# Performance work log

Measured on AMD Instinct MI355X. Metric: run time of the kernel, lower is better.

## Reference

```python
import jax, jax.numpy as jnp
import numpy as np

HEAD_SIZE = 128
ROTARY_DIM = 128
BASE = 10000.0
MAX_POS = 32768
NUM_TOKENS = 8192
NUM_HEADS = 32
NUM_KV_HEADS = 8


def setup_inputs() -> dict:
    key = jax.random.key(0)
    k0, k1, k2, k3 = jax.random.split(key, 4)
    qkv_dim = (NUM_HEADS + 2 * NUM_KV_HEADS) * HEAD_SIZE  # 6144
    qkv = jax.random.normal(k0, (NUM_TOKENS, qkv_dim), dtype=jnp.float32)
    q_weight = jax.random.uniform(k1, (HEAD_SIZE,), dtype=jnp.float32)
    k_weight = jax.random.uniform(k2, (HEAD_SIZE,), dtype=jnp.float32)
    positions = jax.random.randint(k3, (NUM_TOKENS,), 0, MAX_POS)
    return {
        "qkv": qkv,
        "q_weight": q_weight,
        "k_weight": k_weight,
        "positions": positions,
        "num_heads": NUM_HEADS,
        "num_kv_heads": NUM_KV_HEADS,
        "eps": 1e-6,
    }


def _rmsnorm(x, w, eps):
    # per-head RMSNorm over head_size, computed in fp32
    xf = x.astype(jnp.float32)
    inv = jax.lax.rsqrt(jnp.mean(xf * xf, axis=-1, keepdims=True) + eps)
    return (xf * inv * w.astype(jnp.float32)).astype(x.dtype)


def _rope_neox(x, cos, sin):
    # x: [T, H, rotary_dim]; cos/sin: [T, 1, rotary_dim//2]
    half = ROTARY_DIM // 2
    x1, x2 = x[..., :half], x[..., half:]
    return jnp.concatenate([x1 * cos - x2 * sin, x2 * cos + x1 * sin], axis=-1)


def reference(qkv, q_weight, k_weight, positions, num_heads, num_kv_heads, eps):
    T = qkv.shape[0]
    nq, nk = num_heads, num_kv_heads
    q = qkv[:, : nq * HEAD_SIZE].reshape(T, nq, HEAD_SIZE)
    k = qkv[:, nq * HEAD_SIZE : (nq + nk) * HEAD_SIZE].reshape(T, nk, HEAD_SIZE)
    v = qkv[:, (nq + nk) * HEAD_SIZE :]  # untouched

    # position-indexed cos/sin (equivalent to gathering from the cache)
    inv_freq = 1.0 / (BASE ** (jnp.arange(0, ROTARY_DIM, 2, dtype=jnp.float32) / ROTARY_DIM))
    freqs = positions.astype(jnp.float32)[:, None] * inv_freq  # [T, rotary_dim//2]
    cos = jnp.cos(freqs).astype(qkv.dtype)[:, None, :]
    sin = jnp.sin(freqs).astype(qkv.dtype)[:, None, :]

    q = _rope_neox(_rmsnorm(q, q_weight, eps), cos, sin)
    k = _rope_neox(_rmsnorm(k, k_weight, eps), cos, sin)

    return jnp.concatenate([q.reshape(T, -1), k.reshape(T, -1), v], axis=-1)
```

## Files before the change

### kernel.cpp

```cpp
#include <hip/hip_runtime.h>


namespace {

constexpr int kNumQ = 32;
constexpr int kNumK = 8;
constexpr int kHead = 128;
constexpr int kRow  = (kNumQ + 2 * kNumK) * kHead;
constexpr int kHalf = 64;
constexpr int kQK   = kNumQ + kNumK;

__global__ __launch_bounds__(256) void rope_qknorm_kernel(
    const float* __restrict__ qkv,
    const float* __restrict__ qw,
    const float* __restrict__ kw,
    const int* __restrict__ positions,
    float* __restrict__ out) {
  const int t   = blockIdx.x;
  const int tid = threadIdx.x;

  __shared__ float s_cos[kHalf];
  __shared__ float s_sin[kHalf];

  if (tid < kHalf) {
    const double log2b = 13.287712379549449629;
    float p = (float)exp2((double)tid * (log2b / 64.0));
    float inv_freq = 1.0f / p;
    float phase = (float)positions[t] * inv_freq;
    const double two_pi = 6.283185307179586476925286766559;
    float pr = (float)fmod((double)phase, two_pi);
    s_cos[tid] = cosf(pr);
    s_sin[tid] = sinf(pr);
  }
  __syncthreads();

  const int g = tid >> 4;
  const int l = tid & 15;

  const float* row  = qkv + (size_t)t * kRow;
  float*       orow = out + (size_t)t * kRow;

  const float4 cz = *reinterpret_cast<const float4*>(&s_cos[l * 4]);
  const float4 sz = *reinterpret_cast<const float4*>(&s_sin[l * 4]);

  const float4 qw1 = *reinterpret_cast<const float4*>(qw + l * 4);
  const float4 qw2 = *reinterpret_cast<const float4*>(qw + kHalf + l * 4);
  const float4 kw1 = *reinterpret_cast<const float4*>(kw + l * 4);
  const float4 kw2 = *reinterpret_cast<const float4*>(kw + kHalf + l * 4);

  #pragma unroll
  for (int hb = 0; hb < 48; hb += 16) {
    const int h = hb + g;
    const float* hp = row + h * kHead + l * 4;
    const float4 a = *reinterpret_cast<const float4*>(hp);
    const float4 b = *reinterpret_cast<const float4*>(hp + kHalf);
    float* op = orow + h * kHead + l * 4;

    if (h < kQK) {
      const bool isQ = (h < kNumQ);
      const float4 w1 = isQ ? qw1 : kw1;
      const float4 w2 = isQ ? qw2 : kw2;

      float ss = a.x * a.x + a.y * a.y + a.z * a.z + a.w * a.w +
                 b.x * b.x + b.y * b.y + b.z * b.z + b.w * b.w;
      #pragma unroll
      for (int m = 1; m < 16; m <<= 1) ss += __shfl_xor(ss, m, 16);
      const float inv = rsqrtf(ss * (1.0f / 128.0f) + 1e-6f);

      const float y1x = a.x * inv * w1.x, y1y = a.y * inv * w1.y;
      const float y1z = a.z * inv * w1.z, y1w = a.w * inv * w1.w;
      const float y2x = b.x * inv * w2.x, y2y = b.y * inv * w2.y;
      const float y2z = b.z * inv * w2.z, y2w = b.w * inv * w2.w;

      float4 o1, o2;
      o1.x = y1x * cz.x - y2x * sz.x;
      o1.y = y1y * cz.y - y2y * sz.y;
      o1.z = y1z * cz.z - y2z * sz.z;
      o1.w = y1w * cz.w - y2w * sz.w;
      o2.x = y2x * cz.x + y1x * sz.x;
      o2.y = y2y * cz.y + y1y * sz.y;
      o2.z = y2z * cz.z + y1z * sz.z;
      o2.w = y2w * cz.w + y1w * sz.w;
      *reinterpret_cast<float4*>(op)         = o1;
      *reinterpret_cast<float4*>(op + kHalf) = o2;
    } else {
      *reinterpret_cast<float4*>(op)         = a;
      *reinterpret_cast<float4*>(op + kHalf) = b;
    }
  }
}

}

extern "C" void kernel_launch(void* const* d_in, const int* in_sizes, int n_in,
                              void* d_out, int out_size, void* d_ws, size_t ws_size,
                              hipStream_t stream) {
  const float* qkv     = (const float*)d_in[0];
  const float* qw      = (const float*)d_in[1];
  const float* kw      = (const float*)d_in[2];
  const int* positions = (const int*)d_in[3];
  float* out           = (float*)d_out;

  const int tokens = in_sizes[3];
  rope_qknorm_kernel<<<tokens, 256, 0, stream>>>(qkv, qw, kw, positions, out);
}
```

Measured before the change: 339.2 us.

## Precompute RoPE cos/sin table in separate kernel and use persistent grid-stride main kernel

Moves the per-token cos/sin computation out of the main kernel into a separate table kernel that uses all 256 threads per block, and replaces the fmod-based range reduction with a rintf-based one. The main kernel now reads cos/sin from the workspace table with no shared memory or block barrier, and runs as a fixed 2048-block grid looping over tokens. This removes the serialized double-precision trig prologue from every block of the memory-bound kernel. In exchange it adds a second launch, extra table traffic, and hardcodes the token count to 8192.

```diff
diff --git a/kernel.cpp b/kernel.cpp
--- a/kernel.cpp
+++ b/kernel.cpp
@@ -9,83 +9,89 @@
 constexpr int kRow  = (kNumQ + 2 * kNumK) * kHead;
 constexpr int kHalf = 64;
 constexpr int kQK   = kNumQ + kNumK;
+constexpr int kTokens = 8192;
 
-__global__ __launch_bounds__(256) void rope_qknorm_kernel(
+__global__ __launch_bounds__(256) void rope_table_kernel(
+    const int* __restrict__ positions,
+    float* __restrict__ cos_tab,
+    float* __restrict__ sin_tab) {
+  const int idx = blockIdx.x * blockDim.x + threadIdx.x;
+  if (idx >= kTokens * kHalf) return;
+  const int t = idx >> 6;
+  const int i = idx & 63;
+  const double log2b = 13.287712379549449629;
+  const float p = (float)exp2((double)i * (log2b / 64.0));
+  const float inv_freq = 1.0f / p;
+  const float phase = (float)positions[t] * inv_freq;
+  const float k = rintf(phase * 0.15915494309189535f);
+  const double r = (double)phase - (double)k * 6.283185307179586476925287;
+  const float pr = (float)r;
+  cos_tab[idx] = cosf(pr);
+  sin_tab[idx] = sinf(pr);
+}
+
+__global__ __launch_bounds__(256) void rope_main_kernel(
     const float* __restrict__ qkv,
     const float* __restrict__ qw,
     const float* __restrict__ kw,
-    const int* __restrict__ positions,
+    const float* __restrict__ cos_tab,
+    const float* __restrict__ sin_tab,
     float* __restrict__ out) {
-  const int t   = blockIdx.x;
   const int tid = threadIdx.x;
-
-  __shared__ float s_cos[kHalf];
-  __shared__ float s_sin[kHalf];
-
-  if (tid < kHalf) {
-    const double log2b = 13.287712379549449629;
-    float p = (float)exp2((double)tid * (log2b / 64.0));
-    float inv_freq = 1.0f / p;
-    float phase = (float)positions[t] * inv_freq;
-    const double two_pi = 6.283185307179586476925286766559;
-    float pr = (float)fmod((double)phase, two_pi);
-    s_cos[tid] = cosf(pr);
-    s_sin[tid] = sinf(pr);
-  }
-  __syncthreads();
-
   const int g = tid >> 4;
   const int l = tid & 15;
-
-  const float* row  = qkv + (size_t)t * kRow;
-  float*       orow = out + (size_t)t * kRow;
-
-  const float4 cz = *reinterpret_cast<const float4*>(&s_cos[l * 4]);
-  const float4 sz = *reinterpret_cast<const float4*>(&s_sin[l * 4]);
 
   const float4 qw1 = *reinterpret_cast<const float4*>(qw + l * 4);
   const float4 qw2 = *reinterpret_cast<const float4*>(qw + kHalf + l * 4);
   const float4 kw1 = *reinterpret_cast<const float4*>(kw + l * 4);
   const float4 kw2 = *reinterpret_cast<const float4*>(kw + kHalf + l * 4);
 
-  #pragma unroll
-  for (int hb = 0; hb < 48; hb += 16) {
-    const int h = hb + g;
-    const float* hp = row + h * kHead + l * 4;
-    const float4 a = *reinterpret_cast<const float4*>(hp);
-    const float4 b = *reinterpret_cast<const float4*>(hp + kHalf);
-    float* op = orow + h * kHead + l * 4;
+  for (int t = blockIdx.x; t < kTokens; t += gridDim.x) {
+    const float* row  = qkv + (size_t)t * kRow;
+    float*       orow = out + (size_t)t * kRow;
 
-    if (h < kQK) {
-      const bool isQ = (h < kNumQ);
-      const float4 w1 = isQ ? qw1 : kw1;
-      const float4 w2 = isQ ? qw2 : kw2;
+    const float4 cz = *reinterpret_cast<const float4*>(cos_tab + t * kHalf + l * 4);
+    const float4 sz = *reinterpret_cast<const float4*>(sin_tab + t * kHalf + l * 4);
 
-      float ss = a.x * a.x + a.y * a.y + a.z * a.z + a.w * a.w +
-                 b.x * b.x + b.y * b.y + b.z * b.z + b.w * b.w;
-      #pragma unroll
-      for (int m = 1; m < 16; m <<= 1) ss += __shfl_xor(ss, m, 16);
-      const float inv = rsqrtf(ss * (1.0f / 128.0f) + 1e-6f);
+    #pragma unroll
+    for (int hb = 0; hb < 48; hb += 16) {
+      const int h = hb + g;
+      const float* hp = row + h * kHead + l * 4;
+      const float4 a = *reinterpret_cast<const float4*>(hp);
+      const float4 b = *reinterpret_cast<const float4*>(hp + kHalf);
+      float* op = orow + h * kHead + l * 4;
 
-      const float y1x = a.x * inv * w1.x, y1y = a.y * inv * w1.y;
-      const float y1z = a.z * inv * w1.z, y1w = a.w * inv * w1.w;
-      const float y2x = b.x * inv * w2.x, y2y = b.y * inv * w2.y;
-      const float y2z = b.z * inv * w2.z, y2w = b.w * inv * w2.w;
+      if (h < kQK) {
+        const bool isQ = (h < kNumQ);
+        const float4 w1 = isQ ? qw1 : kw1;
+        const float4 w2 = isQ ? qw2 : kw2;
 
-      float4 o1, o2;
-      o1.x = y1x * cz.x - y2x * sz.x;
-      o1.y = y1y * cz.y - y2y * sz.y;
-      o1.z = y1z * cz.z - y2z * sz.z;
-      o1.w = y1w * cz.w - y2w * sz.w;
-      o2.x = y2x * cz.x + y1x * sz.x;
-      o2.y = y2y * cz.y + y1y * sz.y;
-      o2.z = y2z * cz.z + y1z * sz.z;
-      o2.w = y2w * cz.w + y1w * sz.w;
-      *reinterpret_cast<float4*>(op)         = o1;
-      *reinterpret_cast<float4*>(op + kHalf) = o2;
-    } else {
-      *reinterpret_cast<float4*>(op)         = a;
-      *reinterpret_cast<float4*>(op + kHalf) = b;
+        float ss = a.x * a.x + a.y * a.y + a.z * a.z + a.w * a.w +
+                   b.x * b.x + b.y * b.y + b.z * b.z + b.w * b.w;
+        #pragma unroll
+        for (int m = 1; m < 16; m <<= 1) ss += __shfl_xor(ss, m, 16);
+        const float inv = rsqrtf(ss * (1.0f / 128.0f) + 1e-6f);
+
+        const float y1x = a.x * inv * w1.x, y1y = a.y * inv * w1.y;
+        const float y1z = a.z * inv * w1.z, y1w = a.w * inv * w1.w;
+        const float y2x = b.x * inv * w2.x, y2y = b.y * inv * w2.y;
+        const float y2z = b.z * inv * w2.z, y2w = b.w * inv * w2.w;
+
+        float4 o1, o2;
+        o1.x = y1x * cz.x - y2x * sz.x;
+        o1.y = y1y * cz.y - y2y * sz.y;
+        o1.z = y1z * cz.z - y2z * sz.z;
+        o1.w = y1w * cz.w - y2w * sz.w;
+        o2.x = y2x * cz.x + y1x * sz.x;
+        o2.y = y2y * cz.y + y1y * sz.y;
+        o2.z = y2z * cz.z + y1z * sz.z;
+        o2.w = y2w * cz.w + y1w * sz.w;
+        *reinterpret_cast<float4*>(op)         = o1;
+        *reinterpret_cast<float4*>(op + kHalf) = o2;
+      } else {
+        *reinterpret_cast<float4*>(op)         = a;
+        *reinterpret_cast<float4*>(op + kHalf) = b;
+      }
     }
   }
 }
@@ -101,6 +107,12 @@
   const int* positions = (const int*)d_in[3];
   float* out           = (float*)d_out;
 
-  const int tokens = in_sizes[3];
-  rope_qknorm_kernel<<<tokens, 256, 0, stream>>>(qkv, qw, kw, positions, out);
+  float* cos_tab = (float*)d_ws;
+  float* sin_tab = cos_tab + (size_t)kTokens * kHalf;
+
+  const int table_elems = kTokens * kHalf;
+  rope_table_kernel<<<(table_elems + 255) / 256, 256, 0, stream>>>(
+      positions, cos_tab, sin_tab);
+
+  rope_main_kernel<<<2048, 256, 0, stream>>>(qkv, qw, kw, cos_tab, sin_tab, out);
 }
```

New measurement: 352.3 us. 3.9% more time.

## Process four tokens per block, cheaper phase reduction, nontemporal stores

Applied to the files above, without the earlier changes.

Each block now handles four tokens, so all 256 threads compute cos/sin for four tokens in parallel and the weight loads are amortised. The double-precision fmod is replaced by an rint-based range reduction with a single double multiply-subtract. Outputs are written with nontemporal stores to avoid polluting cache. Fewer blocks means less parallelism per block launch, and the new reduction may differ slightly in accuracy for large phases.

```diff
diff --git a/kernel.cpp b/kernel.cpp
--- a/kernel.cpp
+++ b/kernel.cpp
@@ -9,39 +9,50 @@
 constexpr int kRow  = (kNumQ + 2 * kNumK) * kHead;
 constexpr int kHalf = 64;
 constexpr int kQK   = kNumQ + kNumK;
+constexpr int kTPB  = 4;
+
+typedef float f32x4 __attribute__((ext_vector_type(4)));
+
+__device__ __forceinline__ void nt_store4(float* p, float x, float y, float z,
+                                          float w) {
+  f32x4 v;
+  v.x = x; v.y = y; v.z = z; v.w = w;
+  __builtin_nontemporal_store(v, reinterpret_cast<f32x4*>(p));
+}
 
 __global__ __launch_bounds__(256) void rope_qknorm_kernel(
     const float* __restrict__ qkv,
     const float* __restrict__ qw,
     const float* __restrict__ kw,
     const int* __restrict__ positions,
-    float* __restrict__ out) {
-  const int t   = blockIdx.x;
+    float* __restrict__ out,
+    int tokens) {
   const int tid = threadIdx.x;
+  const int t0  = blockIdx.x * kTPB;
 
-  __shared__ float s_cos[kHalf];
-  __shared__ float s_sin[kHalf];
+  __shared__ float s_cos[kTPB][kHalf];
+  __shared__ float s_sin[kTPB][kHalf];
 
-  if (tid < kHalf) {
-    const double log2b = 13.287712379549449629;
-    float p = (float)exp2((double)tid * (log2b / 64.0));
-    float inv_freq = 1.0f / p;
-    float phase = (float)positions[t] * inv_freq;
-    const double two_pi = 6.283185307179586476925286766559;
-    float pr = (float)fmod((double)phase, two_pi);
-    s_cos[tid] = cosf(pr);
-    s_sin[tid] = sinf(pr);
+  {
+    const int tl = tid >> 6;
+    const int i  = tid & 63;
+    const int t  = t0 + tl;
+    if (t < tokens) {
+      const double log2b = 13.287712379549449629;
+      const float p = (float)exp2((double)i * (log2b / 64.0));
+      const float inv_freq = 1.0f / p;
+      const float phase = (float)positions[t] * inv_freq;
+      const float k = rintf(phase * 0.15915494309189535f);
+      const double r = (double)phase - (double)k * 6.283185307179586476925287;
+      const float pr = (float)r;
+      s_cos[tl][i] = cosf(pr);
+      s_sin[tl][i] = sinf(pr);
+    }
   }
   __syncthreads();
 
   const int g = tid >> 4;
   const int l = tid & 15;
-
-  const float* row  = qkv + (size_t)t * kRow;
-  float*       orow = out + (size_t)t * kRow;
-
-  const float4 cz = *reinterpret_cast<const float4*>(&s_cos[l * 4]);
-  const float4 sz = *reinterpret_cast<const float4*>(&s_sin[l * 4]);
 
   const float4 qw1 = *reinterpret_cast<const float4*>(qw + l * 4);
   const float4 qw2 = *reinterpret_cast<const float4*>(qw + kHalf + l * 4);
@@ -49,43 +60,49 @@
   const float4 kw2 = *reinterpret_cast<const float4*>(kw + kHalf + l * 4);
 
   #pragma unroll
-  for (int hb = 0; hb < 48; hb += 16) {
-    const int h = hb + g;
-    const float* hp = row + h * kHead + l * 4;
-    const float4 a = *reinterpret_cast<const float4*>(hp);
-    const float4 b = *reinterpret_cast<const float4*>(hp + kHalf);
-    float* op = orow + h * kHead + l * 4;
+  for (int tl = 0; tl < kTPB; ++tl) {
+    const int t = t0 + tl;
+    if (t >= tokens) break;
+    const float* row  = qkv + (size_t)t * kRow;
+    float*       orow = out + (size_t)t * kRow;
 
-    if (h < kQK) {
-      const bool isQ = (h < kNumQ);
-      const float4 w1 = isQ ? qw1 : kw1;
-      const float4 w2 = isQ ? qw2 : kw2;
+    const float4 cz = *reinterpret_cast<const float4*>(&s_cos[tl][l * 4]);
+    const float4 sz = *reinterpret_cast<const float4*>(&s_sin[tl][l * 4]);
 
-      float ss = a.x * a.x + a.y * a.y + a.z * a.z + a.w * a.w +
-                 b.x * b.x + b.y * b.y + b.z * b.z + b.w * b.w;
-      #pragma unroll
-      for (int m = 1; m < 16; m <<= 1) ss += __shfl_xor(ss, m, 16);
-      const float inv = rsqrtf(ss * (1.0f / 128.0f) + 1e-6f);
+    #pragma unroll
+    for (int hb = 0; hb < 48; hb += 16) {
+      const int h = hb + g;
+      const float* hp = row + h * kHead + l * 4;
+      const float4 a = *reinterpret_cast<const float4*>(hp);
+      const float4 b = *reinterpret_cast<const float4*>(hp + kHalf);
+      float* op = orow + h * kHead + l * 4;
 
-      const float y1x = a.x * inv * w1.x, y1y = a.y * inv * w1.y;
-      const float y1z = a.z * inv * w1.z, y1w = a.w * inv * w1.w;
-      const float y2x = b.x * inv * w2.x, y2y = b.y * inv * w2.y;
-      const float y2z = b.z * inv * w2.z, y2w = b.w * inv * w2.w;
+      if (h < kQK) {
+        const bool isQ = (h < kNumQ);
+        const float4 w1 = isQ ? qw1 : kw1;
+        const float4 w2 = isQ ? qw2 : kw2;
 
-      float4 o1, o2;
-      o1.x = y1x * cz.x - y2x * sz.x;
-      o1.y = y1y * cz.y - y2y * sz.y;
-      o1.z = y1z * cz.z - y2z * sz.z;
-      o1.w = y1w * cz.w - y2w * sz.w;
-      o2.x = y2x * cz.x + y1x * sz.x;
-      o2.y = y2y * cz.y + y1y * sz.y;
-      o2.z = y2z * cz.z + y1z * sz.z;
-      o2.w = y2w * cz.w + y1w * sz.w;
-      *reinterpret_cast<float4*>(op)         = o1;
-      *reinterpret_cast<float4*>(op + kHalf) = o2;
-    } else {
-      *reinterpret_cast<float4*>(op)         = a;
-      *reinterpret_cast<float4*>(op + kHalf) = b;
+        float ss = a.x * a.x + a.y * a.y + a.z * a.z + a.w * a.w +
+                   b.x * b.x + b.y * b.y + b.z * b.z + b.w * b.w;
+        #pragma unroll
+        for (int m = 1; m < 16; m <<= 1) ss += __shfl_xor(ss, m, 16);
+        const float inv = rsqrtf(ss * (1.0f / 128.0f) + 1e-6f);
+
+        const float y1x = a.x * inv * w1.x, y1y = a.y * inv * w1.y;
+        const float y1z = a.z * inv * w1.z, y1w = a.w * inv * w1.w;
+        const float y2x = b.x * inv * w2.x, y2y = b.y * inv * w2.y;
+        const float y2z = b.z * inv * w2.z, y2w = b.w * inv * w2.w;
+
+        nt_store4(op,
+                  y1x * cz.x - y2x * sz.x, y1y * cz.y - y2y * sz.y,
+                  y1z * cz.z - y2z * sz.z, y1w * cz.w - y2w * sz.w);
+        nt_store4(op + kHalf,
+                  y2x * cz.x + y1x * sz.x, y2y * cz.y + y1y * sz.y,
+                  y2z * cz.z + y1z * sz.z, y2w * cz.w + y1w * sz.w);
+      } else {
+        nt_store4(op, a.x, a.y, a.z, a.w);
+        nt_store4(op + kHalf, b.x, b.y, b.z, b.w);
+      }
     }
   }
 }
@@ -102,5 +119,7 @@
   float* out           = (float*)d_out;
 
   const int tokens = in_sizes[3];
-  rope_qknorm_kernel<<<tokens, 256, 0, stream>>>(qkv, qw, kw, positions, out);
+  const int blocks = (tokens + kTPB - 1) / kTPB;
+  rope_qknorm_kernel<<<blocks, 256, 0, stream>>>(qkv, qw, kw, positions, out,
+                                                 tokens);
 }
```

After: 354.9 us. +4.6%, slower.
